# Optimization experiments

Hardware: AMD Instinct MI355X
Metric: run time of the kernel (lower is better)

## Reference

```python
import jax, jax.numpy as jnp
import numpy as np

TOP_K = 8
NUM_EXPERTS = 256
NUM_GROUPS = 8
TOPK_GROUP = 4
SCALE = 2.5
EPS = 1e-20


def setup_inputs() -> dict:
    key = jax.random.key(0)
    k1, k2, k3 = jax.random.split(key, 3)
    T, H = 8192, 7168
    hidden_states = jax.random.normal(k1, (T, H), dtype=jnp.float32)
    # scale ~ kaiming-ish so logits are O(1) and sigmoid is not saturated
    weight = jax.random.normal(k2, (NUM_EXPERTS, H), dtype=jnp.float32) * (H ** -0.5)
    e_score_correction_bias = jax.random.normal(k3, (NUM_EXPERTS,), dtype=jnp.float32) * 0.1
    return {"hidden_states": hidden_states, "weight": weight,
            "e_score_correction_bias": e_score_correction_bias}


def reference(hidden_states, weight, e_score_correction_bias):
    T = hidden_states.shape[0]
    epg = NUM_EXPERTS // NUM_GROUPS  # experts per group
    # gating logits: [T, E]
    logits = jnp.einsum('th,eh->te', hidden_states.astype(jnp.float32),
                        weight.astype(jnp.float32))
    scores = jax.nn.sigmoid(logits)
    scores_for_choice = scores + e_score_correction_bias[None, :]
    # group score = sum of top-2 corrected scores within each group: [T, G]
    grouped = scores_for_choice.reshape(T, NUM_GROUPS, epg)
    top2, _ = jax.lax.top_k(grouped, 2)
    group_scores = top2.sum(axis=-1)
    # select topk_group groups, build mask [T, G]
    _, group_idx = jax.lax.top_k(group_scores, TOPK_GROUP)
    group_mask = jnp.zeros((T, NUM_GROUPS), dtype=scores.dtype)
    group_mask = group_mask.at[jnp.arange(T)[:, None], group_idx].set(1.0)
    # expand to expert mask [T, E]
    score_mask = jnp.repeat(group_mask, epg, axis=1)
    tmp_scores = jnp.where(score_mask > 0, scores_for_choice, 0.0)
    # top_k experts among allowed groups
    _, topk_idx = jax.lax.top_k(tmp_scores, TOP_K)
    # gather UNcorrected scores as weights
    topk_weight = jnp.take_along_axis(scores, topk_idx, axis=1)
    topk_weight = topk_weight / (topk_weight.sum(axis=-1, keepdims=True) + EPS)
    topk_weight = topk_weight * SCALE
    return topk_idx, topk_weight
```

## Files before the change

kernel.cpp:

```cpp
#include <hip/hip_runtime.h>
#include <cmath>

typedef __attribute__((ext_vector_type(8))) _Float16 half8;
typedef __attribute__((ext_vector_type(8))) unsigned short ushort8;
typedef __attribute__((ext_vector_type(4))) float f32x4;

#define HH 7168
#define NE 256
#define NQ 224
#define NITER 112
#define TOPK 8
#define TOPKG 4
#define WSC 1024.f
#define INV_WS (1.f/1024.f)
#define C1 (1.f/2048.f)
#define C2 (1.f/4194304.f)

__device__ __forceinline__ void split2(float x, unsigned short& h, unsigned short& m){
  const _Float16 hh = (_Float16)x;
  const float r = x - (float)hh;
  const _Float16 mm = (_Float16)(r * 2048.f);
  h = __builtin_bit_cast(unsigned short, hh);
  m = __builtin_bit_cast(unsigned short, mm);
}

__global__ __launch_bounds__(256) void prep_w(const float* __restrict__ wgt,
                                              unsigned short* __restrict__ bh,
                                              unsigned short* __restrict__ bm){
  const int b = blockIdx.x;
  const int nt = b & 15, qb = (b >> 4) * 4;
  const int w = threadIdx.x >> 6, L = threadIdx.x & 63;
  const int q = qb + w;
  const int e = nt*16 + (L & 15);
  const int k0 = 32*q + 8*(L >> 4);
  const float4 a0 = *(const float4*)(wgt + (size_t)e*HH + k0);
  const float4 a1 = *(const float4*)(wgt + (size_t)e*HH + k0 + 4);
  const float v[8] = {a0.x,a0.y,a0.z,a0.w,a1.x,a1.y,a1.z,a1.w};
  ushort8 h8, m8;
#pragma unroll
  for(int j=0;j<8;j++){ unsigned short hh,mm; split2(v[j]*WSC, hh, mm); h8[j]=hh; m8[j]=mm; }
  const size_t base = ((size_t)(q*16+nt)*64 + L)*8;
  *(ushort8*)(bh+base) = h8;
  *(ushort8*)(bm+base) = m8;
}

#define AB(aw,lvl,mt,q,row) ((((((aw)*2+(lvl))*4+(mt))*2+(q))*64+(row))*16)
#define BB(lvl,q,nt) ((((lvl)*2+(q))*8+(nt))<<10)
__device__ __forceinline__ int swz(int bo){ return bo ^ (((bo >> 8) & 7) << 4); }

__device__ __forceinline__ void glds16(const void* g, void* l){
  __builtin_amdgcn_global_load_lds(
      (const __attribute__((address_space(1))) unsigned int*)g,
      (__attribute__((address_space(3))) unsigned int*)l, 16, 0, 0);
}

__global__ __launch_bounds__(512,2)
void gemm(const float* __restrict__ hs,
          const unsigned short* __restrict__ bhp,
          const unsigned short* __restrict__ bmp,
          float* __restrict__ lgout){
  __shared__ __align__(16) unsigned char blds[65536];
  __shared__ __align__(16) unsigned char alds[32768];

  const int tid = threadIdx.x, lane = tid & 63, w = tid >> 6;
  const int b = blockIdx.x;
  const int slice = (b >> 2) & 1;
  const int tg = (b >> 3)*4 + (b & 3);
  const int tb = tg*64, eb = slice*128;
  const int mtp = w >> 2, ntp = w & 3;

  f32x4 ksum[2][2], kcmp[2][2], c0[2][2], c1[2][2], c2[2][2];
#pragma unroll
  for(int a=0;a<2;a++)
#pragma unroll
    for(int c=0;c<2;c++){ ksum[a][c]=f32x4{0,0,0,0}; kcmp[a][c]=f32x4{0,0,0,0}; }

  const int tokS = tid >> 3, kidx = tid & 7;
  const int mtS = tokS >> 4, m16S = tokS & 15;
  const int qS = kidx >> 2, kgS = kidx & 3;
  const int rowS = kgS*16 + m16S;
  const float* agp = hs + (size_t)(tb + tokS)*HH + kidx*8;
  float4 ga[2];

  auto stage = [&](int aw){
    unsigned short h[8], m[8];
    const float* gv = (const float*)ga;
#pragma unroll
    for(int p=0;p<8;p++) split2(gv[p], h[p], m[p]);
    ushort8 h8, m8;
#pragma unroll
    for(int j=0;j<8;j++){ h8[j]=h[j]; m8[j]=m[j]; }
    *(ushort8*)&alds[swz(AB(aw,0,mtS,qS,rowS))] = h8;
    *(ushort8*)&alds[swz(AB(aw,1,mtS,qS,rowS))] = m8;
  };

  auto bstage = [&](int bufoff, int inext){
#pragma unroll
    for(int j=0;j<4;j++){
      const int sid = w*4 + j;
      const int lvl = sid >> 4, q = (sid >> 3) & 1, nt = sid & 7;
      const int q32 = 2*inext + q;
      const unsigned short* src = (lvl ? bmp : bhp)
          + ((size_t)((q32*16 + slice*8 + nt)*64 + lane))*8;
      glds16(src, &blds[bufoff + BB(lvl,q,nt)]);
    }
  };

  auto compute = [&](int aw, int s, int bbuf){
    half8 ah[2], am[2];
#pragma unroll
    for(int mtl=0;mtl<2;mtl++){
      const int mt = mtp*2 + mtl;
      ah[mtl] = *(const half8*)&alds[swz(AB(aw,0,mt,s,lane))];
      am[mtl] = *(const half8*)&alds[swz(AB(aw,1,mt,s,lane))];
    }
    half8 Bh[2], Bm[2];
#pragma unroll
    for(int ntl=0;ntl<2;ntl++){
      Bh[ntl] = *(const half8*)&blds[bbuf + BB(0,s,ntp*2+ntl) + lane*16];
      Bm[ntl] = *(const half8*)&blds[bbuf + BB(1,s,ntp*2+ntl) + lane*16];
    }
    __builtin_amdgcn_s_setprio(1);
#pragma unroll
    for(int mtl=0;mtl<2;mtl++)
#pragma unroll
      for(int ntl=0;ntl<2;ntl++){
        c0[mtl][ntl] = __builtin_amdgcn_mfma_f32_16x16x32_f16(ah[mtl], Bh[ntl], c0[mtl][ntl], 0,0,0);
        c1[mtl][ntl] = __builtin_amdgcn_mfma_f32_16x16x32_f16(ah[mtl], Bm[ntl], c1[mtl][ntl], 0,0,0);
        c1[mtl][ntl] = __builtin_amdgcn_mfma_f32_16x16x32_f16(am[mtl], Bh[ntl], c1[mtl][ntl], 0,0,0);
        c2[mtl][ntl] = __builtin_amdgcn_mfma_f32_16x16x32_f16(am[mtl], Bm[ntl], c2[mtl][ntl], 0,0,0);
      }
    __builtin_amdgcn_s_setprio(0);
  };

  ga[0] = *(const float4*)agp;
  ga[1] = *(const float4*)(agp + 4);
  bstage(0, 0);
  stage(0);
  __syncthreads();

#pragma unroll 1
  for(int i=0;i<NITER;i++){
    const int cur = i & 1, nb = cur ^ 1;
    const bool more = (i+1 < NITER);
    if(more){
      const float* ap = agp + (size_t)(i+1)*64;
      ga[0] = *(const float4*)ap;
      ga[1] = *(const float4*)(ap + 4);
      bstage(nb*32768, i+1);
    }
    if((i & 1) == 0){
#pragma unroll
      for(int a=0;a<2;a++)
#pragma unroll
        for(int c=0;c<2;c++){ c0[a][c]=f32x4{0,0,0,0}; c1[a][c]=f32x4{0,0,0,0}; c2[a][c]=f32x4{0,0,0,0}; }
    }
    compute(cur, 0, cur*32768);
    compute(cur, 1, cur*32768);
    if(more) stage(nb);
    if(i & 1){
#pragma unroll
      for(int a=0;a<2;a++)
#pragma unroll
        for(int c=0;c<2;c++)
#pragma unroll
          for(int r=0;r<4;r++){
            const float v = c0[a][c][r] + c1[a][c][r]*C1 + c2[a][c][r]*C2;
            const float y = v - kcmp[a][c][r];
            const float t = ksum[a][c][r] + y;
            kcmp[a][c][r] = (t - ksum[a][c][r]) - y;
            ksum[a][c][r] = t;
          }
    }
    __syncthreads();
  }

#pragma unroll
  for(int mtl=0;mtl<2;mtl++)
#pragma unroll
    for(int ntl=0;ntl<2;ntl++)
#pragma unroll
      for(int r=0;r<4;r++){
        const int tok = (mtp*2+mtl)*16 + (lane>>4)*4 + r;
        const int e = (ntp*2+ntl)*16 + (lane&15);
        const float lg = (ksum[mtl][ntl][r] - kcmp[mtl][ntl][r]) * INV_WS;
        lgout[(size_t)(tb+tok)*NE + eb + e] = lg;
      }
}

__global__ __launch_bounds__(256)
void gate(const float* __restrict__ lg, const float* __restrict__ bias,
          float* __restrict__ out, int T){
  const int tid = threadIdx.x, lane = tid & 63, wv = tid >> 6;
  const int t = blockIdx.x*4 + wv;
  const float4 bias4 = *(const float4*)(bias + 4*lane);
  const int g = lane >> 3;
  const float NEG_INF = -__builtin_inff();

  const float4 l4 = *(const float4*)(lg + (size_t)t*NE + 4*lane);
  float4 r4;
  r4.x = 1.f/(1.f + expf(-l4.x));
  r4.y = 1.f/(1.f + expf(-l4.y));
  r4.z = 1.f/(1.f + expf(-l4.z));
  r4.w = 1.f/(1.f + expf(-l4.w));
  float4 s4;
  s4.x = r4.x + bias4.x; s4.y = r4.y + bias4.y;
  s4.z = r4.z + bias4.z; s4.w = r4.w + bias4.w;

  float m1 = s4.x, m2 = NEG_INF;
  if (s4.y > m1) { m2 = m1; m1 = s4.y; } else if (s4.y > m2) m2 = s4.y;
  if (s4.z > m1) { m2 = m1; m1 = s4.z; } else if (s4.z > m2) m2 = s4.z;
  if (s4.w > m1) { m2 = m1; m1 = s4.w; } else if (s4.w > m2) m2 = s4.w;
#pragma unroll
  for (int m = 1; m <= 4; m <<= 1) {
    const float o1 = __shfl_xor(m1, m);
    const float o2 = __shfl_xor(m2, m);
    const float nm1 = fmaxf(m1, o1);
    const float nm2 = fmaxf(fminf(m1, o1), fmaxf(m2, o2));
    m1 = nm1; m2 = nm2;
  }
  const float gs = m1 + m2;

  float gsv[8];
#pragma unroll
  for (int j = 0; j < 8; ++j) gsv[j] = __shfl(gs, j * 8);

  unsigned gm = 0;
#pragma unroll
  for (int r = 0; r < TOPKG; ++r) {
    float best = NEG_INF; int bj = 0;
#pragma unroll
    for (int j = 0; j < 8; ++j) {
      const bool avail = !((gm >> j) & 1u);
      if (avail && gsv[j] > best) { best = gsv[j]; bj = j; }
    }
    gm |= 1u << bj;
  }
  const bool allowed = (gm >> g) & 1u;

  float v0 = allowed ? s4.x : 0.f;
  float v1 = allowed ? s4.y : 0.f;
  float v2 = allowed ? s4.z : 0.f;
  float v3 = allowed ? s4.w : 0.f;

  float sumw = 0.f;
  int myidx = 0; float myraw = 0.f;
#pragma unroll
  for (int r = 0; r < TOPK; ++r) {
    float bv = v0; int bj = 0;
    if (v1 > bv) { bv = v1; bj = 1; }
    if (v2 > bv) { bv = v2; bj = 2; }
    if (v3 > bv) { bv = v3; bj = 3; }
    int bidx = 4 * lane + bj;
#pragma unroll
    for (int m = 1; m < 64; m <<= 1) {
      const float ov = __shfl_xor(bv, m);
      const int   oi = __shfl_xor(bidx, m);
      if (ov > bv || (ov == bv && oi < bidx)) { bv = ov; bidx = oi; }
    }
    const int oj = bidx & 3;
    const float cand = (oj == 0) ? r4.x
                     : (oj == 1) ? r4.y
                     : (oj == 2) ? r4.z
                     :             r4.w;
    const float raw = __shfl(cand, bidx >> 2);
    sumw += raw;
    if (lane == r) { myidx = bidx; myraw = raw; }
    if (lane == (bidx >> 2)) {
      if      (oj == 0) v0 = NEG_INF;
      else if (oj == 1) v1 = NEG_INF;
      else if (oj == 2) v2 = NEG_INF;
      else              v3 = NEG_INF;
    }
  }

  if (lane < TOPK) {
    out[(size_t)t * TOPK + lane] = (float)myidx;
    out[(size_t)T * TOPK + (size_t)t * TOPK + lane] = myraw / (sumw + 1e-20f) * 2.5f;
  }
}

extern "C" void kernel_launch(void* const* d_in, const int* in_sizes, int n_in,
                              void* d_out, int out_size, void* d_ws, size_t ws_size,
                              hipStream_t stream) {
  const float* hs   = (const float*)d_in[0];
  const float* wgt  = (const float*)d_in[1];
  const float* bias = (const float*)d_in[2];
  float* out = (float*)d_out;

  const int T = in_sizes[0] / HH;

  unsigned short* bh = (unsigned short*)d_ws;
  unsigned short* bm = bh + (size_t)NE*HH;
  float* lgbuf = (float*)(bm + (size_t)NE*HH);

  hipLaunchKernelGGL(prep_w, dim3(896), dim3(256), 0, stream, wgt, bh, bm);
  hipLaunchKernelGGL(gemm,   dim3(256), dim3(512), 0, stream, hs, bh, bm, lgbuf);
  hipLaunchKernelGGL(gate,   dim3(T/4), dim3(256), 0, stream, lgbuf, bias, out, T);
}
```

Before: 497.3 us.

## Halve B staging granularity to cut LDS and raise occupancy hint

The main loop now stages the B operand one 32-wide K slice per iteration instead of two, which halves the B shared buffer from 64KB to 32KB. The loop runs twice as many iterations: A is still staged per 64-wide window, and the compensated-sum flush now happens every four iterations. Launch bounds are raised to request four blocks per CU, aiming to overlap more waves through higher occupancy. In exchange there are twice as many barriers and less work per barrier, and the tighter register budget may cause spills.

Result: slower. 597.6 us (+20.2%).

```diff
diff --git a/kernel.cpp b/kernel.cpp
--- a/kernel.cpp
+++ b/kernel.cpp
@@ -8,7 +8,8 @@
 #define HH 7168
 #define NE 256
 #define NQ 224
-#define NITER 112
+#define NITER 224
+#define NWIN 112
 #define TOPK 8
 #define TOPKG 4
 #define WSC 1024.f
@@ -45,7 +46,7 @@
 }
 
 #define AB(aw,lvl,mt,q,row) ((((((aw)*2+(lvl))*4+(mt))*2+(q))*64+(row))*16)
-#define BB(lvl,q,nt) ((((lvl)*2+(q))*8+(nt))<<10)
+#define BB32(lvl,nt) (((lvl)*8+(nt))<<10)
 __device__ __forceinline__ int swz(int bo){ return bo ^ (((bo >> 8) & 7) << 4); }
 
 __device__ __forceinline__ void glds16(const void* g, void* l){
@@ -54,12 +55,12 @@
       (__attribute__((address_space(3))) unsigned int*)l, 16, 0, 0);
 }
 
-__global__ __launch_bounds__(512,2)
+__global__ __launch_bounds__(512,4)
 void gemm(const float* __restrict__ hs,
           const unsigned short* __restrict__ bhp,
           const unsigned short* __restrict__ bmp,
           float* __restrict__ lgout){
-  __shared__ __align__(16) unsigned char blds[65536];
+  __shared__ __align__(16) unsigned char blds[32768];
   __shared__ __align__(16) unsigned char alds[32768];
 
   const int tid = threadIdx.x, lane = tid & 63, w = tid >> 6;
@@ -94,31 +95,30 @@
     *(ushort8*)&alds[swz(AB(aw,1,mtS,qS,rowS))] = m8;
   };
 
-  auto bstage = [&](int bufoff, int inext){
-#pragma unroll
-    for(int j=0;j<4;j++){
-      const int sid = w*4 + j;
-      const int lvl = sid >> 4, q = (sid >> 3) & 1, nt = sid & 7;
-      const int q32 = 2*inext + q;
+  auto bstage = [&](int bufoff, int q32){
+#pragma unroll
+    for(int j=0;j<2;j++){
+      const int sid = w*2 + j;
+      const int lvl = sid >> 3, nt = sid & 7;
       const unsigned short* src = (lvl ? bmp : bhp)
           + ((size_t)((q32*16 + slice*8 + nt)*64 + lane))*8;
-      glds16(src, &blds[bufoff + BB(lvl,q,nt)]);
+      glds16(src, &blds[bufoff + BB32(lvl,nt)]);
     }
   };
 
-  auto compute = [&](int aw, int s, int bbuf){
+  auto compute = [&](int aw, int qh, int bbuf){
     half8 ah[2], am[2];
 #pragma unroll
     for(int mtl=0;mtl<2;mtl++){
       const int mt = mtp*2 + mtl;
-      ah[mtl] = *(const half8*)&alds[swz(AB(aw,0,mt,s,lane))];
-      am[mtl] = *(const half8*)&alds[swz(AB(aw,1,mt,s,lane))];
+      ah[mtl] = *(const half8*)&alds[swz(AB(aw,0,mt,qh,lane))];
+      am[mtl] = *(const half8*)&alds[swz(AB(aw,1,mt,qh,lane))];
     }
     half8 Bh[2], Bm[2];
 #pragma unroll
     for(int ntl=0;ntl<2;ntl++){
-      Bh[ntl] = *(const half8*)&blds[bbuf + BB(0,s,ntp*2+ntl) + lane*16];
-      Bm[ntl] = *(const half8*)&blds[bbuf + BB(1,s,ntp*2+ntl) + lane*16];
+      Bh[ntl] = *(const half8*)&blds[bbuf + BB32(0,ntp*2+ntl) + lane*16];
+      Bm[ntl] = *(const half8*)&blds[bbuf + BB32(1,ntp*2+ntl) + lane*16];
     }
     __builtin_amdgcn_s_setprio(1);
 #pragma unroll
@@ -141,24 +141,27 @@
 
 #pragma unroll 1
   for(int i=0;i<NITER;i++){
-    const int cur = i & 1, nb = cur ^ 1;
-    const bool more = (i+1 < NITER);
-    if(more){
-      const float* ap = agp + (size_t)(i+1)*64;
+    const int wnd = i >> 1, qh = i & 1;
+    const int aw = wnd & 1;
+    const int bcur = (i & 1) ? 16384 : 0;
+    const bool moreB = (i+1 < NITER);
+    const bool moreA = (wnd+1 < NWIN);
+
+    if(moreB) bstage(bcur ^ 16384, i+1);
+    if(qh == 0 && moreA){
+      const float* ap = agp + (size_t)(wnd+1)*64;
       ga[0] = *(const float4*)ap;
       ga[1] = *(const float4*)(ap + 4);
-      bstage(nb*32768, i+1);
-    }
-    if((i & 1) == 0){
+    }
+    if((i & 3) == 0){
 #pragma unroll
       for(int a=0;a<2;a++)
 #pragma unroll
         for(int c=0;c<2;c++){ c0[a][c]=f32x4{0,0,0,0}; c1[a][c]=f32x4{0,0,0,0}; c2[a][c]=f32x4{0,0,0,0}; }
     }
-    compute(cur, 0, cur*32768);
-    compute(cur, 1, cur*32768);
-    if(more) stage(nb);
-    if(i & 1){
+    compute(aw, qh, bcur);
+    if(qh == 1 && moreA) stage(aw ^ 1);
+    if((i & 3) == 3){
 #pragma unroll
       for(int a=0;a<2;a++)
 #pragma unroll
```
